# Kernel optimization log

Hardware: AMD Instinct MI355X
Metric: run time of the kernel (lower is better)

The kernel has to match this reference:

```python
import jax, jax.numpy as jnp
import numpy as np

BATCH, N, D, N_STEPS = 16, 128, 128, 5
EPS = 1e-10

def setup_inputs() -> dict:
    key = jax.random.key(0)
    k1, k2 = jax.random.split(key)
    x = jax.random.normal(k1, (BATCH, D), dtype=jnp.float32)
    L = jax.random.normal(k2, (N, D, D), dtype=jnp.float32) * 0.1
    temperature = jnp.array(1.0, dtype=jnp.float32)
    target_similarity = jnp.array(-0.5, dtype=jnp.float32)
    step_size = jnp.array(0.1, dtype=jnp.float32)
    return {"x": x, "L": L, "temperature": temperature,
            "target_similarity": target_similarity, "step_size": step_size}

def _bases(L):
    # Cayley transform per bubble: U = (I + A)^{-1} (I - A), A skew-symmetric
    A = L - jnp.swapaxes(L, -1, -2)               # [N, d, d]
    I = jnp.eye(L.shape[-1], dtype=L.dtype)
    return jnp.linalg.solve(I[None] + A, I[None] - A)  # [N, d, d]

def reference(x, L, temperature, target_similarity, step_size):
    n = L.shape[0]
    bases = _bases(L)                              # [N, d, d]

    # measurements[b, i] = x[b] @ U_i
    measurements = jnp.einsum('bd,ndk->bnk', x, bases)  # [B, N, d]

    # surface tension: pairwise Frobenius distance between bases
    diff_b = bases[None, :] - bases[:, None]       # [N, N, d, d]
    tension = jnp.sqrt(jnp.sum(diff_b ** 2, axis=(-2, -1)) + 1e-8)  # [N, N]

    temp = jnp.maximum(jnp.abs(temperature), 0.01)
    interaction = jax.nn.softmax(-tension / temp, axis=-1)  # [N, N]
    mask = 1.0 - jnp.eye(n, dtype=x.dtype)
    w = (mask * interaction)[None]                 # [1, N, N]
    step = jnp.clip(jnp.abs(step_size), 0.001, 0.5)

    state = measurements
    for _ in range(N_STEPS):
        state_n = state / (jnp.linalg.norm(state, axis=-1, keepdims=True) + EPS)
        cos_sim = jnp.einsum('bnd,bmd->bnm', state_n, state_n)   # [B, N, N]
        force_mag = (cos_sim - target_similarity) * w            # [B, N, N]
        diff = state[:, :, None, :] - state[:, None, :, :]       # [B, N, N, d]
        diff_n = diff / (jnp.linalg.norm(diff, axis=-1, keepdims=True) + EPS)
        forces = jnp.einsum('bnm,bnmd->bnd', force_mag, diff_n)  # [B, N, d]
        state = state + step * forces
    equilibrium = state

    # expressions[b, i] = equilibrium[b, i] @ U_i^T
    expressions = jnp.einsum('bnd,nkd->bnk', equilibrium, bases)

    # density matrix per batch element
    m_norm = equilibrium / (jnp.linalg.norm(equilibrium, axis=-1, keepdims=True) + EPS)
    rho = jnp.einsum('bnd,bne->bde', m_norm, m_norm) / n         # [B, d, d]
    eigenvalues = jnp.linalg.eigvalsh(rho)                        # [B, d]
    eigenvalues = jnp.maximum(eigenvalues, 1e-12)
    output_dist = eigenvalues / jnp.sum(eigenvalues, axis=-1, keepdims=True)

    output_avg = jnp.mean(expressions, axis=1)                   # [B, d]
    return (output_avg, output_dist, rho, measurements, equilibrium,
            expressions, tension)
```

## Files before the change

kernel.cpp:

```cpp
#include <hip/hip_runtime.h>

#define EPSF 1e-10f

__device__ __forceinline__ float f4sel(float4 a, int cc) {
  float r = (cc == 0) ? a.x : a.y;
  r = (cc == 2) ? a.z : r;
  r = (cc == 3) ? a.w : r;
  return r;
}

__device__ __forceinline__ float dpp_quad_sum(float x) {
  x += __int_as_float(__builtin_amdgcn_update_dpp(
      0, __float_as_int(x), 0xB1, 0xf, 0xf, true));
  x += __int_as_float(__builtin_amdgcn_update_dpp(
      0, __float_as_int(x), 0x4E, 0xf, 0xf, true));
  return x;
}

__device__ __forceinline__ float dpp_red_sum64(float x) {
  x += __int_as_float(__builtin_amdgcn_update_dpp(0, __float_as_int(x), 0x111, 0xf, 0xf, true));
  x += __int_as_float(__builtin_amdgcn_update_dpp(0, __float_as_int(x), 0x112, 0xf, 0xf, true));
  x += __int_as_float(__builtin_amdgcn_update_dpp(0, __float_as_int(x), 0x114, 0xf, 0xe, true));
  x += __int_as_float(__builtin_amdgcn_update_dpp(0, __float_as_int(x), 0x118, 0xf, 0xc, true));
  x += __int_as_float(__builtin_amdgcn_update_dpp(0, __float_as_int(x), 0x142, 0xa, 0xf, true));
  x += __int_as_float(__builtin_amdgcn_update_dpp(0, __float_as_int(x), 0x143, 0xc, 0xf, true));
  return __int_as_float(__builtin_amdgcn_readlane(__float_as_int(x), 63));
}

#define SWZ4(i, j4) ((i) * 32 + ((j4) ^ ((i) & 31)))
#define SWZF(i, j) (SWZ4((i), (j) >> 2) * 4 + ((j) & 3))

__global__ __launch_bounds__(512, 2) void k_cayley(const float* __restrict__ L,
                                                   float* __restrict__ bases) {
  extern __shared__ float4 sm4[];
  float4* M4  = sm4;
  float*  Mf  = (float*)M4;
  float4* rb0 = sm4 + 4096;
  float4* rb1 = rb0 + 32;
  float*  cb0 = (float*)(rb1 + 32);
  float*  cb1 = cb0 + 128;
  const int n = blockIdx.x, t = threadIdx.x;
  const float* Ln = L + n * 16384;
  for (int f = t; f < 4096; f += 512) {
    int i = f >> 5, j4 = f & 31;
    M4[SWZ4(i, j4)] = ((const float4*)Ln)[f];
  }
  __syncthreads();
  for (int f = t; f < 16384; f += 512) {
    int i = f >> 7, j = f & 127;
    if (i < j) {
      int a = SWZF(i, j), b = SWZF(j, i);
      float va = Mf[a], vb = Mf[b];
      Mf[a] = va - vb;
      Mf[b] = vb - va;
    } else if (i == j) {
      Mf[SWZF(i, i)] = 1.0f;
    }
  }
  __syncthreads();
  const int i = t & 127;
  const int h2 = t >> 7;
  float4 Ar[8];
  #pragma unroll
  for (int u = 0; u < 8; ++u) Ar[u] = M4[SWZ4(i, h2 * 8 + u)];
  if (i == 0) {
    #pragma unroll
    for (int u = 0; u < 8; ++u) rb0[h2 * 8 + u] = Ar[u];
  }
  if (h2 == 0) cb0[i] = Ar[0].x;
  __syncthreads();
  for (int k = 0; k < 128; ++k) {
    const float4* rbC = (k & 1) ? rb1 : rb0;
    float4*       rbN = (k & 1) ? rb0 : rb1;
    const float*  cbC = (k & 1) ? cb1 : cb0;
    float*        cbN = (k & 1) ? cb0 : cb1;
    const float pivinv = 1.0f / cbC[k];
    const float coef = cbC[i] * pivinv;
    const int kj4 = k >> 2, kc = k & 3;
    const int nj4 = (k + 1) >> 2, ncc = (k + 1) & 3;
    const bool isPiv = (i == k);
    const bool isNext = (i == k + 1);
    float colv = 0.0f;
    #pragma unroll
    for (int u = 0; u < 8; ++u) {
      const int jj = h2 * 8 + u;
      float4 r = rbC[jj];
      float4 a;
      if (isPiv) {
        a.x = r.x * pivinv; a.y = r.y * pivinv;
        a.z = r.z * pivinv; a.w = r.w * pivinv;
        if (jj == kj4) {
          a.x = (kc == 0) ? pivinv : a.x;
          a.y = (kc == 1) ? pivinv : a.y;
          a.z = (kc == 2) ? pivinv : a.z;
          a.w = (kc == 3) ? pivinv : a.w;
        }
      } else {
        a = Ar[u];
        a.x -= coef * r.x; a.y -= coef * r.y;
        a.z -= coef * r.z; a.w -= coef * r.w;
        if (jj == kj4) {
          a.x = (kc == 0) ? -coef : a.x;
          a.y = (kc == 1) ? -coef : a.y;
          a.z = (kc == 2) ? -coef : a.z;
          a.w = (kc == 3) ? -coef : a.w;
        }
      }
      Ar[u] = a;
      if (jj == nj4) colv = f4sel(a, ncc);
      if (isNext) rbN[jj] = a;
    }
    if (h2 == (nj4 >> 3)) cbN[i] = colv;
    __syncthreads();
  }
  #pragma unroll
  for (int u = 0; u < 8; ++u) M4[SWZ4(i, h2 * 8 + u)] = Ar[u];
  __syncthreads();
  for (int f = t; f < 16384; f += 512) {
    int ii = f >> 7, j = f & 127;
    float v = Mf[SWZF(ii, j)];
    bases[n * 16384 + f] = 2.0f * v - ((ii == j) ? 1.0f : 0.0f);
  }
}

__global__ __launch_bounds__(256) void k_gramp(const float* __restrict__ bases,
                                               float* __restrict__ part) {
  __shared__ __align__(16) float tile[64][132];
  const int b = blockIdx.x, t = threadIdx.x;
  const int tx = t & 15, ty = t >> 4;
  const int i0 = tx * 8, j0 = ty * 8;
  const int k0 = b * 512;
  float acc[8][8];
  #pragma unroll
  for (int u = 0; u < 8; ++u)
    #pragma unroll
    for (int v = 0; v < 8; ++v) acc[u][v] = 0.f;
  for (int c0 = 0; c0 < 512; c0 += 64) {
    __syncthreads();
    for (int f = t; f < 8192; f += 256) {
      int i = f >> 6, kk = f & 63;
      tile[kk][i] = bases[i * 16384 + k0 + c0 + kk];
    }
    __syncthreads();
    for (int kk = 0; kk < 64; ++kk) {
      float4 a0 = *(const float4*)&tile[kk][i0];
      float4 a1 = *(const float4*)&tile[kk][i0 + 4];
      float4 b0 = *(const float4*)&tile[kk][j0];
      float4 b1 = *(const float4*)&tile[kk][j0 + 4];
      float av[8] = {a0.x, a0.y, a0.z, a0.w, a1.x, a1.y, a1.z, a1.w};
      float bv[8] = {b0.x, b0.y, b0.z, b0.w, b1.x, b1.y, b1.z, b1.w};
      #pragma unroll
      for (int u = 0; u < 8; ++u)
        #pragma unroll
        for (int v = 0; v < 8; ++v) acc[u][v] += av[u] * bv[v];
    }
  }
  float* P = part + b * 16384;
  #pragma unroll
  for (int u = 0; u < 8; ++u) {
    #pragma unroll
    for (int v4 = 0; v4 < 2; ++v4) {
      float4 o;
      o.x = acc[u][v4 * 4 + 0]; o.y = acc[u][v4 * 4 + 1];
      o.z = acc[u][v4 * 4 + 2]; o.w = acc[u][v4 * 4 + 3];
      *(float4*)&P[(i0 + u) * 128 + j0 + v4 * 4] = o;
    }
  }
}

__global__ __launch_bounds__(256) void k_gsum(const float* __restrict__ part,
                                              float* __restrict__ G) {
  const int g = blockIdx.x * 256 + threadIdx.x;
  float s = 0.f;
  for (int p = 0; p < 32; ++p) s += part[p * 16384 + g];
  G[g] = s;
}

__global__ __launch_bounds__(128) void k_wsoft(const float* __restrict__ G,
                                               const float* __restrict__ temp_p,
                                               float* __restrict__ w,
                                               float* __restrict__ tension_out) {
  const int i = blockIdx.x, t = threadIdx.x;
  __shared__ float rr[2], r2[2];
  float temp = fmaxf(fabsf(*temp_p), 0.01f);
  float gii = G[i * 128 + i], gjj = G[t * 128 + t], gij = G[i * 128 + t];
  float ten = sqrtf(fmaxf(gii + gjj - 2.0f * gij, 0.0f) + 1e-8f);
  tension_out[i * 128 + t] = ten;
  float logit = -ten / temp;
  float m = logit;
  for (int s = 32; s > 0; s >>= 1) m = fmaxf(m, __shfl_xor(m, s));
  if ((t & 63) == 0) rr[t >> 6] = m;
  __syncthreads();
  float mx = fmaxf(rr[0], rr[1]);
  float ex = expf(logit - mx);
  float ssum = ex;
  for (int s = 32; s > 0; s >>= 1) ssum += __shfl_xor(ssum, s);
  if ((t & 63) == 0) r2[t >> 6] = ssum;
  __syncthreads();
  float tot = r2[0] + r2[1];
  float wv = ex / tot;
  if (t == i) wv = 0.0f;
  w[i * 128 + t] = wv;
}

__global__ __launch_bounds__(128) void k_meas(const float* __restrict__ x,
                                              const float* __restrict__ bases,
                                              float* __restrict__ meas_out,
                                              float* __restrict__ state0,
                                              float* __restrict__ norms0) {
  const int n = blockIdx.x, t = threadIdx.x;
  __shared__ float xs[2048];
  __shared__ float red[2];
  for (int f = t; f < 2048; f += 128) xs[f] = x[f];
  __syncthreads();
  float acc[16];
  #pragma unroll
  for (int b = 0; b < 16; ++b) acc[b] = 0.f;
  for (int d = 0; d < 128; ++d) {
    float u = bases[n * 16384 + d * 128 + t];
    #pragma unroll
    for (int b = 0; b < 16; ++b) acc[b] += xs[b * 128 + d] * u;
  }
  for (int b = 0; b < 16; ++b) {
    meas_out[(b * 128 + n) * 128 + t] = acc[b];
    state0[(b * 128 + n) * 128 + t] = acc[b];
  }
  for (int b = 0; b < 16; ++b) {
    float v = acc[b] * acc[b];
    for (int s = 32; s > 0; s >>= 1) v += __shfl_down(v, s);
    if ((t & 63) == 0) red[t >> 6] = v;
    __syncthreads();
    if (t == 0) norms0[b * 128 + n] = sqrtf(red[0] + red[1]);
    __syncthreads();
  }
}

__global__ __launch_bounds__(128) void k_step(const float* __restrict__ src,
                                              float* __restrict__ dst,
                                              const float* __restrict__ w,
                                              const float* __restrict__ norms_in,
                                              float* __restrict__ norms_out,
                                              const float* __restrict__ tgt_p,
                                              const float* __restrict__ step_p) {
  const int b = blockIdx.x >> 7, n = blockIdx.x & 127, t = threadIdx.x;
  __shared__ float sn[128];
  __shared__ __align__(16) float chunk[32][132];
  __shared__ float red[2][32];
  __shared__ float cbuf[32];
  __shared__ float red2[2];
  const float target = *tgt_p;
  const float step = fminf(fmaxf(fabsf(*step_p), 0.001f), 0.5f);
  const float* srcb = src + b * 16384;
  float x_d = srcb[n * 128 + t];
  sn[t] = x_d;
  float norm_n = norms_in[b * 128 + n];
  float nn2 = norm_n * norm_n;
  float f_d = 0.0f;
  __syncthreads();
  for (int c0 = 0; c0 < 128; c0 += 32) {
    for (int f = t; f < 1024; f += 128) {
      int row = f >> 5, c4 = f & 31;
      ((float4*)&chunk[row][0])[c4] =
          ((const float4*)(srcb + (c0 + row) * 128))[c4];
    }
    __syncthreads();
    int m = t & 31, q = t >> 5;
    float dp = 0.f;
    const float* cr = &chunk[m][0];
    #pragma unroll
    for (int i2 = 0; i2 < 32; ++i2) {
      int dd = q * 32 + i2;
      dp += cr[dd] * sn[dd];
    }
    dp += __shfl_xor(dp, 32);
    int wave = t >> 6;
    if ((t & 63) < 32) red[wave][m] = dp;
    __syncthreads();
    if (t < 32) {
      float dot = red[0][t] + red[1][t];
      int mm = c0 + t;
      float norm_m = norms_in[b * 128 + mm];
      float sq = nn2 + norm_m * norm_m - 2.0f * dot;
      float wnm = w[n * 128 + mm];
      float cs = dot / ((norm_n + EPSF) * (norm_m + EPSF));
      float fm = (cs - target) * wnm;
      cbuf[t] = fm / (sqrtf(fmaxf(sq, 0.0f)) + EPSF);
    }
    __syncthreads();
    #pragma unroll
    for (int mi = 0; mi < 32; ++mi) f_d += cbuf[mi] * (x_d - chunk[mi][t]);
    __syncthreads();
  }
  float nv = x_d + step * f_d;
  dst[(b * 128 + n) * 128 + t] = nv;
  float v = nv * nv;
  for (int s = 32; s > 0; s >>= 1) v += __shfl_down(v, s);
  if ((t & 63) == 0) red2[t >> 6] = v;
  __syncthreads();
  if (t == 0) norms_out[b * 128 + n] = sqrtf(red2[0] + red2[1]);
}

__global__ __launch_bounds__(128) void k_expr(const float* __restrict__ eq,
                                              const float* __restrict__ bases,
                                              float* __restrict__ expr_out) {
  const int n = blockIdx.x, t = threadIdx.x;
  __shared__ __align__(16) float es[16][128];
  for (int f = t; f < 2048; f += 128)
    es[f >> 7][f & 127] = eq[((f >> 7) * 128 + n) * 128 + (f & 127)];
  __syncthreads();
  float acc[16];
  #pragma unroll
  for (int b = 0; b < 16; ++b) acc[b] = 0.f;
  const float4* U = (const float4*)(bases + n * 16384 + t * 128);
  for (int d4 = 0; d4 < 32; ++d4) {
    float4 u = U[d4];
    #pragma unroll
    for (int b = 0; b < 16; ++b) {
      float4 e4 = ((const float4*)&es[b][0])[d4];
      acc[b] += u.x * e4.x + u.y * e4.y + u.z * e4.z + u.w * e4.w;
    }
  }
  for (int b = 0; b < 16; ++b) expr_out[(b * 128 + n) * 128 + t] = acc[b];
}

__global__ __launch_bounds__(128) void k_avg(const float* __restrict__ expr,
                                             float* __restrict__ avg) {
  const int b = blockIdx.x, t = threadIdx.x;
  float s = 0.f;
  for (int n = 0; n < 128; ++n) s += expr[(b * 128 + n) * 128 + t];
  avg[b * 128 + t] = s * (1.0f / 128.0f);
}

__global__ __launch_bounds__(256) void k_rho(const float* __restrict__ eq,
                                             const float* __restrict__ norms,
                                             float* __restrict__ rho) {
  const int b = blockIdx.x >> 3, dt = blockIdx.x & 7;
  const int t = threadIdx.x;
  __shared__ float ch[32][129];
  int e = t & 127, dl = t >> 7;
  float acc[8];
  #pragma unroll
  for (int o = 0; o < 8; ++o) acc[o] = 0.f;
  for (int c0 = 0; c0 < 128; c0 += 32) {
    for (int f = t; f < 4096; f += 256) {
      int row = f >> 7, col = f & 127;
      int nn = c0 + row;
      float inv = 1.0f / (norms[b * 128 + nn] + EPSF);
      ch[row][col] = eq[(b * 128 + nn) * 128 + col] * inv;
    }
    __syncthreads();
    for (int nn = 0; nn < 32; ++nn) {
      float me = ch[nn][e];
      #pragma unroll
      for (int o = 0; o < 8; ++o) {
        int d = dt * 16 + dl + o * 2;
        acc[o] += ch[nn][d] * me;
      }
    }
    __syncthreads();
  }
  for (int o = 0; o < 8; ++o) {
    int d = dt * 16 + dl + o * 2;
    rho[(b * 128 + d) * 128 + e] = acc[o] * (1.0f / 128.0f);
  }
}

__global__ __launch_bounds__(512, 1) void k_tridiag(const float* __restrict__ rho,
                                                    float* __restrict__ dvec_g,
                                                    float* __restrict__ evec_g) {
  __shared__ __align__(16) float cb0[128];
  __shared__ __align__(16) float cb1[128];
  __shared__ __align__(16) float pbuf[128];
  __shared__ float dvl[128], evl[128];
  __shared__ float redS[8], redK[8], redX[1];
  const int bb = blockIdx.x, t = threadIdx.x;
  const int i = t >> 2, h = t & 3, wv = t >> 6;
  const float* R = rho + bb * 16384;
  float4 Ar[8];
  const float4* Rp = (const float4*)(R + i * 128 + h * 32);
  #pragma unroll
  for (int u = 0; u < 8; ++u) Ar[u] = Rp[u];
  if (h == 0) {
    cb0[i] = (i == 0) ? 0.f : Ar[0].x;
    if (i == 0) dvl[0] = Ar[0].x;
    if (i == 1) redX[0] = Ar[0].x;
  }
  {
    float s2w = dpp_red_sum64((h == 0 && i > 0) ? Ar[0].x * Ar[0].x : 0.f);
    if ((t & 63) == 0) redS[wv] = s2w;
  }
  __syncthreads();
  for (int k = 0; k < 126; ++k) {
    const float* cbC = (k & 1) ? cb1 : cb0;
    float*       cbN = (k & 1) ? cb0 : cb1;
    float sig2 = redS[0] + redS[1] + redS[2] + redS[3] +
                 redS[4] + redS[5] + redS[6] + redS[7];
    float x0 = redX[0];
    const bool skip = (sig2 < 1e-30f);
    float sig = sqrtf(sig2);
    float alpha = (x0 >= 0.f) ? -sig : sig;
    if (skip) alpha = 0.f;
    float beta = skip ? 0.f : 1.f / (sig2 - alpha * x0);
    float w0 = x0 - alpha;
    if (t == 0) evl[k] = alpha;
    const int jn4 = (k + 1) >> 2, ncc = (k + 1) & 3, hn = (k + 1) >> 5;
    float vt = (i == k + 1) ? w0 : cbC[i];
    const float4* cv4 = (const float4*)cbC;
    float pp = 0.f;
    #pragma unroll
    for (int u = 0; u < 8; ++u) {
      const int jj = h * 8 + u;
      float4 v = cv4[jj];
      if (jj == jn4) {
        v.x = (0 == ncc) ? w0 : v.x;
        v.y = (1 == ncc) ? w0 : v.y;
        v.z = (2 == ncc) ? w0 : v.z;
        v.w = (3 == ncc) ? w0 : v.w;
      }
      pp += Ar[u].x * v.x + Ar[u].y * v.y + Ar[u].z * v.z + Ar[u].w * v.w;
    }
    pp = dpp_quad_sum(pp);
    float p = beta * pp;
    if (i <= k) p = 0.f;
    if (h == 0) pbuf[i] = p;
    float kpw = dpp_red_sum64((h == 0) ? vt * p : 0.f);
    if ((t & 63) == 0) redK[wv] = kpw;
    __syncthreads();
    float K = (redK[0] + redK[1] + redK[2] + redK[3] +
               redK[4] + redK[5] + redK[6] + redK[7]) * beta * 0.5f;
    float cn = 0.f;
    if (i > k) {
      float qt = p - K * vt;
      const float4* pv4 = (const float4*)pbuf;
      #pragma unroll
      for (int u = 0; u < 8; ++u) {
        const int jj = h * 8 + u;
        float4 v = cv4[jj];
        if (jj == jn4) {
          v.x = (0 == ncc) ? w0 : v.x;
          v.y = (1 == ncc) ? w0 : v.y;
          v.z = (2 == ncc) ? w0 : v.z;
          v.w = (3 == ncc) ? w0 : v.w;
        }
        float4 pq = pv4[jj];
        float qx = pq.x - K * v.x, qy = pq.y - K * v.y;
        float qz = pq.z - K * v.z, qw = pq.w - K * v.w;
        Ar[u].x -= vt * qx + qt * v.x;
        Ar[u].y -= vt * qy + qt * v.y;
        Ar[u].z -= vt * qz + qt * v.z;
        Ar[u].w -= vt * qw + qt * v.w;
        if (jj == jn4) cn = f4sel(Ar[u], ncc);
      }
    }
    if (h == hn) cbN[i] = (i <= k + 1) ? 0.f : cn;
    if (i == k + 1 && h == hn) dvl[k + 1] = cn;
    if (i == k + 2 && h == hn) redX[0] = cn;
    float s2w = dpp_red_sum64((h == hn && i > k + 1) ? cn * cn : 0.f);
    if ((t & 63) == 0) redS[wv] = s2w;
    __syncthreads();
  }
  if (i == 126 && h == 3) dvl[126] = Ar[7].z;
  if (i == 127 && h == 3) { evl[126] = Ar[7].z; dvl[127] = Ar[7].w; }
  if (t == 0) evl[127] = 0.0f;
  __syncthreads();
  if (t < 128) {
    dvec_g[bb * 128 + t] = dvl[t];
    evec_g[bb * 128 + t] = evl[t];
  }
}

__global__ __launch_bounds__(1024, 1) void k_bisect(const float* __restrict__ dvec_g,
                                                    const float* __restrict__ evec_g,
                                                    float* __restrict__ dist_out) {
  const int bb = blockIdx.x, t = threadIdx.x;
  const int idx = t >> 3;
  const int c = t & 7;
  __shared__ float ds[128], e2s[128], eabs[128];
  __shared__ float lam[128];
  __shared__ float rr[2];
  if (t < 128) {
    ds[t] = dvec_g[bb * 128 + t];
    float e = evec_g[bb * 128 + t];
    e2s[t] = e * e;
    eabs[t] = fabsf(e);
  }
  __syncthreads();
  float lo = 1e30f, hi = -1e30f;
  for (int ii = 0; ii < 128; ++ii) {
    float r = (ii > 0 ? eabs[ii - 1] : 0.0f) + (ii < 127 ? eabs[ii] : 0.0f);
    lo = fminf(lo, ds[ii] - r);
    hi = fmaxf(hi, ds[ii] + r);
  }
  const float frac = (float)(c + 1) * (1.0f / 9.0f);
  for (int it = 0; it < 13; ++it) {
    float mid = lo + (hi - lo) * frac;
    int cnt = 0;
    float q = ds[0] - mid;
    if (q < 0.0f) cnt++;
    for (int ii = 1; ii < 128; ++ii) {
      float denom = q;
      if (fabsf(denom) < 1e-25f) denom = (denom < 0.0f) ? -1e-25f : 1e-25f;
      q = (ds[ii] - mid) - __fdividef(e2s[ii - 1], denom);
      if (q < 0.0f) cnt++;
    }
    bool isLo = (cnt <= idx);
    float cl = isLo ? mid : -1e30f;
    float ch = isLo ? 1e30f : mid;
    #pragma unroll
    for (int s = 1; s < 8; s <<= 1) {
      cl = fmaxf(cl, __shfl_xor(cl, s));
      ch = fminf(ch, __shfl_xor(ch, s));
    }
    lo = fmaxf(lo, cl);
    hi = fminf(hi, ch);
  }
  if (c == 0) lam[idx] = 0.5f * (lo + hi);
  __syncthreads();
  if (t < 128) {
    float evc = fmaxf(lam[t], 1e-12f);
    float ssum = evc;
    for (int s = 32; s > 0; s >>= 1) ssum += __shfl_xor(ssum, s);
    if ((t & 63) == 0) rr[t >> 6] = ssum;
    __syncthreads();
    float tot = rr[0] + rr[1];
    dist_out[bb * 128 + t] = evc / tot;
  } else {
    __syncthreads();
  }
}

extern "C" void kernel_launch(void* const* d_in, const int* in_sizes, int n_in,
                              void* d_out, int out_size, void* d_ws, size_t ws_size,
                              hipStream_t stream) {
  const float* x      = (const float*)d_in[0];
  const float* L      = (const float*)d_in[1];
  const float* temp_p = (const float*)d_in[2];
  const float* tgt_p  = (const float*)d_in[3];
  const float* step_p = (const float*)d_in[4];
  float* out = (float*)d_out;
  float* ws  = (float*)d_ws;

  float* bases = ws;
  float* G     = bases + 2097152;
  float* w     = G + 16384;
  float* s0    = w + 16384;
  float* s1    = s0 + 262144;
  float* n0    = s1 + 262144;
  float* n1    = n0 + 2048;
  float* dv    = n1 + 2048;
  float* ev    = dv + 2048;

  float* gpart = s0;

  float* o_avg  = out;
  float* o_dist = out + 2048;
  float* o_rho  = out + 4096;
  float* o_meas = out + 266240;
  float* o_eq   = out + 528384;
  float* o_expr = out + 790528;
  float* o_ten  = out + 1052672;

  hipFuncSetAttribute((const void*)k_cayley,
                      hipFuncAttributeMaxDynamicSharedMemorySize, 67584);

  k_cayley<<<128, 512, 67584, stream>>>(L, bases);
  k_gramp<<<32, 256, 0, stream>>>(bases, gpart);
  k_gsum<<<64, 256, 0, stream>>>(gpart, G);
  k_wsoft<<<128, 128, 0, stream>>>(G, temp_p, w, o_ten);
  k_meas<<<128, 128, 0, stream>>>(x, bases, o_meas, s0, n0);
  k_step<<<2048, 128, 0, stream>>>(s0, s1, w, n0, n1, tgt_p, step_p);
  k_step<<<2048, 128, 0, stream>>>(s1, s0, w, n1, n0, tgt_p, step_p);
  k_step<<<2048, 128, 0, stream>>>(s0, s1, w, n0, n1, tgt_p, step_p);
  k_step<<<2048, 128, 0, stream>>>(s1, s0, w, n1, n0, tgt_p, step_p);
  k_step<<<2048, 128, 0, stream>>>(s0, o_eq, w, n0, n1, tgt_p, step_p);
  k_expr<<<128, 128, 0, stream>>>(o_eq, bases, o_expr);
  k_avg<<<16, 128, 0, stream>>>(o_expr, o_avg);
  k_rho<<<128, 256, 0, stream>>>(o_eq, n1, o_rho);
  k_tridiag<<<16, 512, 0, stream>>>(o_rho, dv, ev);
  k_bisect<<<16, 1024, 0, stream>>>(dv, ev, o_dist);
}
```

Baseline: 859.1 us.

## Split eigenvalue bisection across more blocks with wider multisection and fewer iterations

The bisection kernel now runs two blocks per batch element, each handling 64 eigenvalues. Each eigenvalue gets 16 probe threads instead of 8, so 8 multisection iterations replace 13 while still narrowing the interval to float precision. The Gershgorin bounds are now computed with a parallel shuffle reduction, and the diagonal and squared off-diagonal are packed as float2 for the Sturm count loop. Normalising the eigenvalues moves to a separate small kernel, which adds one launch and a round trip through global memory.

Result: faster. 790.2 us, median of 3 (-8.0%).

```diff
diff --git a/kernel.cpp b/kernel.cpp
--- a/kernel.cpp
+++ b/kernel.cpp
@@ -471,62 +471,80 @@
 
 __global__ __launch_bounds__(1024, 1) void k_bisect(const float* __restrict__ dvec_g,
                                                     const float* __restrict__ evec_g,
-                                                    float* __restrict__ dist_out) {
-  const int bb = blockIdx.x, t = threadIdx.x;
-  const int idx = t >> 3;
-  const int c = t & 7;
-  __shared__ float ds[128], e2s[128], eabs[128];
-  __shared__ float lam[128];
-  __shared__ float rr[2];
+                                                    float* __restrict__ lam_g) {
+  const int bb = blockIdx.x >> 1, half = blockIdx.x & 1;
+  const int t = threadIdx.x;
+  const int idx = half * 64 + (t >> 4);
+  const int c = t & 15;
+  __shared__ __align__(8) float2 de[130];
+  __shared__ float eabs_s[128];
+  __shared__ float redlo[2], redhi[2];
   if (t < 128) {
-    ds[t] = dvec_g[bb * 128 + t];
+    float d = dvec_g[bb * 128 + t];
     float e = evec_g[bb * 128 + t];
-    e2s[t] = e * e;
-    eabs[t] = fabsf(e);
-  }
-  __syncthreads();
-  float lo = 1e30f, hi = -1e30f;
-  for (int ii = 0; ii < 128; ++ii) {
-    float r = (ii > 0 ? eabs[ii - 1] : 0.0f) + (ii < 127 ? eabs[ii] : 0.0f);
-    lo = fminf(lo, ds[ii] - r);
-    hi = fmaxf(hi, ds[ii] + r);
-  }
-  const float frac = (float)(c + 1) * (1.0f / 9.0f);
-  for (int it = 0; it < 13; ++it) {
+    de[t].x = d;
+    de[t + 1].y = e * e;
+    eabs_s[t] = fabsf(e);
+    if (t == 0) {
+      de[0].y = 0.f;
+      de[128].x = 0.f;
+      de[129] = make_float2(0.f, 0.f);
+    }
+  }
+  __syncthreads();
+  if (t < 128) {
+    float d = de[t].x;
+    float r = ((t > 0) ? eabs_s[t - 1] : 0.f) + ((t < 127) ? eabs_s[t] : 0.f);
+    float lo_t = d - r, hi_t = d + r;
+    for (int s = 32; s > 0; s >>= 1) {
+      lo_t = fminf(lo_t, __shfl_xor(lo_t, s));
+      hi_t = fmaxf(hi_t, __shfl_xor(hi_t, s));
+    }
+    if ((t & 63) == 0) { redlo[t >> 6] = lo_t; redhi[t >> 6] = hi_t; }
+  }
+  __syncthreads();
+  float lo = fminf(redlo[0], redlo[1]);
+  float hi = fmaxf(redhi[0], redhi[1]);
+  const float frac = (float)(c + 1) * (1.0f / 17.0f);
+  for (int it = 0; it < 8; ++it) {
     float mid = lo + (hi - lo) * frac;
-    int cnt = 0;
-    float q = ds[0] - mid;
-    if (q < 0.0f) cnt++;
+    float q = de[0].x - mid;
+    int cnt = (q < 0.0f) ? 1 : 0;
+    float2 c0v = de[1], c1v = de[2];
+    #pragma unroll 2
     for (int ii = 1; ii < 128; ++ii) {
+      float2 nx = de[ii + 2];
       float denom = q;
       if (fabsf(denom) < 1e-25f) denom = (denom < 0.0f) ? -1e-25f : 1e-25f;
-      q = (ds[ii] - mid) - __fdividef(e2s[ii - 1], denom);
-      if (q < 0.0f) cnt++;
+      q = (c0v.x - mid) - __fdividef(c0v.y, denom);
+      cnt += (q < 0.0f) ? 1 : 0;
+      c0v = c1v; c1v = nx;
     }
     bool isLo = (cnt <= idx);
     float cl = isLo ? mid : -1e30f;
     float ch = isLo ? 1e30f : mid;
     #pragma unroll
-    for (int s = 1; s < 8; s <<= 1) {
+    for (int s = 1; s < 16; s <<= 1) {
       cl = fmaxf(cl, __shfl_xor(cl, s));
       ch = fminf(ch, __shfl_xor(ch, s));
     }
     lo = fmaxf(lo, cl);
     hi = fminf(hi, ch);
   }
-  if (c == 0) lam[idx] = 0.5f * (lo + hi);
-  __syncthreads();
-  if (t < 128) {
-    float evc = fmaxf(lam[t], 1e-12f);
-    float ssum = evc;
-    for (int s = 32; s > 0; s >>= 1) ssum += __shfl_xor(ssum, s);
-    if ((t & 63) == 0) rr[t >> 6] = ssum;
-    __syncthreads();
-    float tot = rr[0] + rr[1];
-    dist_out[bb * 128 + t] = evc / tot;
-  } else {
-    __syncthreads();
-  }
+  if (c == 0) lam_g[bb * 128 + idx] = 0.5f * (lo + hi);
+}
+
+__global__ __launch_bounds__(128) void k_dist(const float* __restrict__ lam_g,
+                                              float* __restrict__ dist_out) {
+  const int bb = blockIdx.x, t = threadIdx.x;
+  __shared__ float rr[2];
+  float evc = fmaxf(lam_g[bb * 128 + t], 1e-12f);
+  float ssum = evc;
+  for (int s = 32; s > 0; s >>= 1) ssum += __shfl_xor(ssum, s);
+  if ((t & 63) == 0) rr[t >> 6] = ssum;
+  __syncthreads();
+  float tot = rr[0] + rr[1];
+  dist_out[bb * 128 + t] = evc / tot;
 }
 
 extern "C" void kernel_launch(void* const* d_in, const int* in_sizes, int n_in,
@@ -549,6 +567,7 @@
   float* n1    = n0 + 2048;
   float* dv    = n1 + 2048;
   float* ev    = dv + 2048;
+  float* lamg  = ev + 2048;
 
   float* gpart = s0;
 
@@ -577,5 +596,6 @@
   k_avg<<<16, 128, 0, stream>>>(o_expr, o_avg);
   k_rho<<<128, 256, 0, stream>>>(o_eq, n1, o_rho);
   k_tridiag<<<16, 512, 0, stream>>>(o_rho, dv, ev);
-  k_bisect<<<16, 1024, 0, stream>>>(dv, ev, o_dist);
-}
+  k_bisect<<<32, 1024, 0, stream>>>(dv, ev, lamg);
+  k_dist<<<16, 128, 0, stream>>>(lamg, o_dist);
+}
```
